# Optimization experiments

Hardware: AMD Instinct MI355X
Metric: run time of the kernel (lower is better)

Reference implementation:

```python
import jax, jax.numpy as jnp
import numpy as np

N, S, H, FA = 16, 64, 256, 256  # batch, sentences, memory_size, fact_attn_hidden


def setup_inputs() -> dict:
    key = jax.random.key(0)
    ks = jax.random.split(key, 12)
    g = lambda k, shp: (jax.random.normal(k, shp, jnp.float32) * 0.05)
    return dict(
        facts=jax.random.normal(ks[0], (N, S, H), jnp.float32),
        prevM=jax.random.normal(ks[1], (N, S, H), jnp.float32),
        questions=jax.random.normal(ks[2], (N, S, H), jnp.float32),
        doc_len=jax.random.randint(ks[3], (N,), S // 2, S + 1),
        z1_w=g(ks[4], (FA, 4 * H)), z1_b=jnp.zeros((FA,), jnp.float32),
        z2_w=g(ks[5], (1, FA)), z2_b=jnp.zeros((1,), jnp.float32),
        Wr_w=g(ks[6], (H, H)), Wr_b=jnp.zeros((H,), jnp.float32),
        Ur_w=g(ks[7], (H, H)), Ur_b=jnp.zeros((H,), jnp.float32),
        W_w=g(ks[8], (H, H)), W_b=jnp.zeros((H,), jnp.float32),
        U_w=g(ks[9], (H, H)), U_b=jnp.zeros((H,), jnp.float32),
        nm_w=g(ks[10], (H, 3 * H)), nm_b=jnp.zeros((H,), jnp.float32),
    )


def reference(facts, prevM, questions, doc_len,
              z1_w, z1_b, z2_w, z2_b,
              Wr_w, Wr_b, Ur_w, Ur_b, W_w, W_b, U_w, U_b,
              nm_w, nm_b):
    n, s, h = facts.shape
    # ---- make_interaction: pairwise features (query axis = dim1, fact/key axis = dim2)
    f = facts[:, None, :, :]       # (N,1,S,H) broadcast over queries
    m = prevM[:, :, None, :]       # (N,S,1,H) broadcast over keys
    q = questions[:, :, None, :]   # (N,S,1,H)
    z = jnp.concatenate([f * q, f * m, jnp.abs(f - q), jnp.abs(f - m)], axis=-1)  # (N,S,S,4H)
    Gh = jnp.tanh(z @ z1_w.T + z1_b)               # (N,S,S,FA)
    G = (Gh @ z2_w.T + z2_b)[..., 0]               # (N,S,S)
    mask = (jnp.arange(s) < doc_len[:, None]).astype(G.dtype)  # (N,S) key mask
    Gm = G * mask[:, None, :]
    Gm = jnp.where(Gm == 0, -jnp.inf, Gm)          # faithful to G[G==0] = -inf
    attn = jax.nn.softmax(Gm, axis=2)              # (N,S,S)

    # ---- AttentionalGRU over the S facts for each of the N*S query rows
    B = n * s
    fb = jnp.broadcast_to(facts[:, None], (n, s, s, h)).reshape(B, s, h)  # (B,S,H)
    gb = attn.reshape(B, s)                                               # (B,S)

    def step(C, xs):
        fact, gt = xs                                   # fact: (B,H), gt: (B,)
        r = jax.nn.sigmoid(fact @ Wr_w.T + Wr_b + C @ Ur_w.T + Ur_b)
        h_t = jnp.tanh(fact @ W_w.T + W_b + r * (C @ U_w.T + U_b))
        gt = gt[:, None]
        return gt * h_t + (1.0 - gt) * C, None

    C0 = jnp.zeros((B, h), facts.dtype)
    C, _ = jax.lax.scan(step, C0, (fb.transpose(1, 0, 2), gb.T))  # scan over S steps
    C = C.reshape(n, s, h)

    # ---- memory update (dropouts are identity in eval mode)
    concat = jnp.concatenate([prevM, C, questions], axis=-1)  # (N,S,3H)
    next_mem = jax.nn.relu(concat @ nm_w.T + nm_b)            # (N,S,H)
    return next_mem, attn
```

## Files before the change

kernel.cpp:

```cpp
#include <hip/hip_runtime.h>
#include <hip/hip_bf16.h>
#include <math.h>

#define NB 16
#define SS 64
#define HH 256
#define FAA 256

using short8 = __attribute__((ext_vector_type(8))) short;
using f32x4  = __attribute__((ext_vector_type(4))) float;

__device__ __forceinline__ unsigned int cvtpk(float a, float b) {
  unsigned int r;
  asm("v_cvt_pk_bf16_f32 %0, %1, %2" : "=v"(r) : "v"(a), "v"(b));
  return r;
}
__device__ __forceinline__ float sel4(const f32x4 a, int q) {
  const float s01 = (q & 1) ? a[1] : a[0];
  const float s23 = (q & 1) ? a[3] : a[2];
  return (q & 2) ? s23 : s01;
}

__global__ __launch_bounds__(256) void prolog_fused(
    const float* __restrict__ z1w, const float* __restrict__ Ur,
    const float* __restrict__ U, const float* __restrict__ nmw,
    const float* __restrict__ pm, const float* __restrict__ qs,
    unsigned short* __restrict__ z1wbf, unsigned short* __restrict__ wcatbf,
    unsigned short* __restrict__ nmbf, unsigned short* __restrict__ pmbf,
    unsigned short* __restrict__ qbf,
    const float* __restrict__ facts, const float* __restrict__ Wr,
    const float* __restrict__ Wrb, const float* __restrict__ Urb,
    const float* __restrict__ Ww, const float* __restrict__ Wb,
    float* __restrict__ FWr, float* __restrict__ FW) {
  __shared__ float fl[4][HH];
  const int bid = blockIdx.x, tid = threadIdx.x;

  auto cvt8 = [&](const float* src, unsigned short* dst, int base) {
    const float4 a = *(const float4*)(src + base);
    const float4 b = *(const float4*)(src + base + 4);
    uint4 o;
    o.x = cvtpk(a.x, a.y); o.y = cvtpk(a.z, a.w);
    o.z = cvtpk(b.x, b.y); o.w = cvtpk(b.z, b.w);
    *(uint4*)(dst + base) = o;
  };
  auto cvt8perm = [&](const float* row, unsigned short* dst, int sbase, int c0) {
    const float4 lo = *(const float4*)(row + c0);
    const float4 hi = *(const float4*)(row + c0 + 16);
    uint4 o;
    o.x = cvtpk(lo.x, hi.x); o.y = cvtpk(lo.y, hi.y);
    o.z = cvtpk(lo.z, hi.z); o.w = cvtpk(lo.w, hi.w);
    *(uint4*)(dst + sbase) = o;
  };

  if (bid < 128) {
    const int base = (bid * 256 + tid) * 8;
    cvt8(z1w, z1wbf, base);
    return;
  }
  if (bid < 192) {
    const int base = ((bid - 128) * 256 + tid) * 8;
    const int o = base >> 8, s0 = base & 255;
    const int gb = s0 & ~31, t0 = s0 & 31;
    const float* row = (o < 256) ? (Ur + o * 256) : (U + (o - 256) * 256);
    cvt8perm(row, wcatbf, base, gb + (t0 >> 1));
    return;
  }
  if (bid < 288) {
    const int base = ((bid - 192) * 256 + tid) * 8;
    const int o = base / 768, k0 = base - o * 768;
    const float* row = nmw + o * 768;
    if (k0 >= 256 && k0 < 512) {
      const int s0 = k0 - 256, gb = s0 & ~31, t0 = s0 & 31;
      cvt8perm(row, nmbf, base, 256 + gb + (t0 >> 1));
    } else {
      cvt8(row, nmbf + o * 768, k0);
    }
    return;
  }
  if (bid < 416) {
    const int base = ((bid - 288) * 256 + tid) * 8;
    cvt8(pm, pmbf, base);
    return;
  }
  if (bid < 544) {
    const int base = ((bid - 416) * 256 + tid) * 8;
    cvt8(qs, qbf, base);
    return;
  }
  const int b0 = (bid - 544) * 4;
#pragma unroll
  for (int r = 0; r < 4; ++r) fl[r][tid] = facts[(b0 + r) * HH + tid];
  __syncthreads();
  float ar[4] = {0.f, 0.f, 0.f, 0.f}, aw[4] = {0.f, 0.f, 0.f, 0.f};
  const float4* wr = (const float4*)(Wr + tid * HH);
  const float4* ww = (const float4*)(Ww + tid * HH);
  for (int d4 = 0; d4 < 64; ++d4) {
    float4 a = wr[d4], b = ww[d4];
#pragma unroll
    for (int r = 0; r < 4; ++r) {
      float4 f = *(const float4*)&fl[r][d4 * 4];
      ar[r] += a.x * f.x + a.y * f.y + a.z * f.z + a.w * f.w;
      aw[r] += b.x * f.x + b.y * f.y + b.z * f.z + b.w * f.w;
    }
  }
  const float br = Wrb[tid] + Urb[tid], bw = Wb[tid];
#pragma unroll
  for (int r = 0; r < 4; ++r) {
    FWr[(b0 + r) * HH + tid] = ar[r] + br;
    FW[(b0 + r) * HH + tid] = aw[r] + bw;
  }
}

__global__ __launch_bounds__(512, 4) void gate_gemm(
    const float* __restrict__ facts, const float* __restrict__ prevM,
    const float* __restrict__ questions, const unsigned short* __restrict__ z1wbf,
    const float* __restrict__ z1b, const float* __restrict__ z2w,
    const float* __restrict__ z2b, const int* __restrict__ doc_len,
    float* __restrict__ attn) {
  __shared__ unsigned short Ab[3][128 * 32];
  __shared__ unsigned short Bb[3][256 * 32];
  __shared__ float Gpart[128][4];

  const int bi = blockIdx.x;
  const int n = bi >> 5, i0 = (bi & 31) * 2;
  const int tid = threadIdx.x;
  const int w = tid >> 6, l = tid & 63;
  const int rg = w >> 2, cg = w & 3;
  const int l15 = l & 15, q = l >> 4;
  const int t15 = tid & 15, jb = tid >> 4;

  const float* fn = facts + n * SS * HH;
  const float* qn = questions + (n * SS + i0) * HH;
  const float* mn = prevM + (n * SS + i0) * HH;

  auto stageB = [&](int buf, int c) {
    const int kb = (c & 3) * 256 + (c >> 2) * 32;
    const int swz = ((l & 3) ^ ((l >> 2) & 3)) * 8;
#pragma unroll
    for (int j = 0; j < 2; ++j) {
      const int colg = w * 32 + j * 16 + (l >> 2);
      const unsigned short* src = z1wbf + colg * 1024 + kb + swz;
      __builtin_amdgcn_global_load_lds(src, Bb[buf] + (w * 32 + j * 16) * 32, 16, 0, 0);
    }
  };

  auto buildA = [&](int buf, int s, float2 f0, float2 f1, float2 q0, float2 q1,
                    float2 m0, float2 m1) {
    unsigned int* dst = (unsigned int*)Ab[buf];
    const int dsw = t15 ^ ((jb & 3) << 2);
    const float2 o0 = (s & 1) ? m0 : q0;
    const float2 o1 = (s & 1) ? m1 : q1;
#pragma unroll
    for (int pl = 0; pl < 2; ++pl) {
      const float fx = pl ? f1.x : f0.x;
      const float fy = pl ? f1.y : f0.y;
#pragma unroll
      for (int il = 0; il < 2; ++il) {
        const int row = il * 64 + pl * 32 + jb;
        const float ox = il ? o1.x : o0.x;
        const float oy = il ? o1.y : o0.y;
        float a, b;
        if (s < 2) { a = fx * ox;         b = fy * oy; }
        else       { a = fabsf(fx - ox);  b = fabsf(fy - oy); }
        dst[row * 16 + dsw] = cvtpk(a, b);
      }
    }
  };

  const f32x4 zero4 = {0.f, 0.f, 0.f, 0.f};
  f32x4 acc[4][4];
#pragma unroll
  for (int a = 0; a < 4; ++a)
#pragma unroll
    for (int b = 0; b < 4; ++b) acc[a][b] = zero4;

  auto mfmaStep = [&](int buf) {
    short8 Bfr[4];
#pragma unroll
    for (int nf = 0; nf < 4; ++nf) {
      const int col = cg * 64 + nf * 16 + l15;
      Bfr[nf] = *(const short8*)&Bb[buf][col * 32 + (q ^ (l15 & 3)) * 8];
    }
    __builtin_amdgcn_s_setprio(1);
#pragma unroll
    for (int mf = 0; mf < 4; ++mf) {
      const int row = rg * 64 + mf * 16 + l15;
      const short8 Afm = *(const short8*)&Ab[buf][row * 32 + (q ^ (l15 & 3)) * 8];
#pragma unroll
      for (int nf = 0; nf < 4; ++nf)
        acc[mf][nf] = __builtin_amdgcn_mfma_f32_16x16x32_bf16(Afm, Bfr[nf], acc[mf][nf], 0, 0, 0);
    }
    __builtin_amdgcn_s_setprio(0);
  };

  const int hh2 = t15 * 2;
  auto pf = [&](int hc, float2& f0, float2& f1, float2& q0, float2& q1,
                float2& m0, float2& m1) {
    const int h = hc * 32 + hh2;
    f0 = *(const float2*)(fn + jb * HH + h);
    f1 = *(const float2*)(fn + (jb + 32) * HH + h);
    q0 = *(const float2*)(qn + h);
    q1 = *(const float2*)(qn + HH + h);
    m0 = *(const float2*)(mn + h);
    m1 = *(const float2*)(mn + HH + h);
  };

  float2 Rf0, Rf1, Rq0, Rq1, Rm0, Rm1;
  float2 Sf0, Sf1, Sq0, Sq1, Sm0, Sm1;
  pf(0, Rf0, Rf1, Rq0, Rq1, Rm0, Rm1);
  stageB(0, 0);
  stageB(1, 1);
  buildA(0, 0, Rf0, Rf1, Rq0, Rq1, Rm0, Rm1);
  asm volatile("s_waitcnt vmcnt(2) lgkmcnt(0)\n\ts_barrier" ::: "memory");

#pragma unroll
  for (int c = 0; c < 32; ++c) {
    const int s = c & 3, hc = c >> 2;
    const int cb = c % 3, nb2 = (c + 1) % 3, fb = (c + 2) % 3;
    const bool pfphase = (s == 2) && (hc < 7);

    if (c + 2 < 32) stageB(fb, c + 2);
    if (pfphase) pf(hc + 1, Sf0, Sf1, Sq0, Sq1, Sm0, Sm1);
    if (c + 1 < 32) {
      if (((c + 1) & 3) == 0)
        buildA(nb2, 0, Sf0, Sf1, Sq0, Sq1, Sm0, Sm1);
      else
        buildA(nb2, (c + 1) & 3, Rf0, Rf1, Rq0, Rq1, Rm0, Rm1);
    }
    mfmaStep(cb);

    if (c <= 29) {
      if (pfphase)
        asm volatile("s_waitcnt vmcnt(8) lgkmcnt(0)\n\ts_barrier" ::: "memory");
      else
        asm volatile("s_waitcnt vmcnt(2) lgkmcnt(0)\n\ts_barrier" ::: "memory");
    } else if (c == 30) {
      asm volatile("s_waitcnt vmcnt(0) lgkmcnt(0)\n\ts_barrier" ::: "memory");
    }
    if (s == 3) {
      Rf0 = Sf0; Rf1 = Sf1; Rq0 = Sq0; Rq1 = Sq1; Rm0 = Sm0; Rm1 = Sm1;
    }
  }

  float psum[4][4];
#pragma unroll
  for (int mf = 0; mf < 4; ++mf)
#pragma unroll
    for (int v = 0; v < 4; ++v) psum[mf][v] = 0.f;

#pragma unroll
  for (int nf = 0; nf < 4; ++nf) {
    const int k = cg * 64 + nf * 16 + l15;
    const float zb = z1b[k], zw = z2w[k];
#pragma unroll
    for (int mf = 0; mf < 4; ++mf)
#pragma unroll
      for (int v = 0; v < 4; ++v) {
        const float x = acc[mf][nf][v] + zb;
        const float e = __expf(2.f * x);
        const float t = 1.f - 2.f / (e + 1.f);
        psum[mf][v] += zw * t;
      }
  }
#pragma unroll
  for (int d = 1; d < 16; d <<= 1)
#pragma unroll
    for (int mf = 0; mf < 4; ++mf)
#pragma unroll
      for (int v = 0; v < 4; ++v) psum[mf][v] += __shfl_xor(psum[mf][v], d, 64);
  if (l15 == 0) {
#pragma unroll
    for (int mf = 0; mf < 4; ++mf)
#pragma unroll
      for (int v = 0; v < 4; ++v)
        Gpart[rg * 64 + mf * 16 + q * 4 + v][cg] = psum[mf][v];
  }
  __syncthreads();
  if (tid < 128) {
    const float gg = Gpart[tid][0] + Gpart[tid][1] + Gpart[tid][2] + Gpart[tid][3] + z2b[0];
    const int i = i0 + (tid >> 6), j = tid & 63;
    const int dl = doc_len[n];
    const float x = (j < dl && gg != 0.0f) ? gg : -INFINITY;
    float mx = x;
#pragma unroll
    for (int d = 1; d < 64; d <<= 1) mx = fmaxf(mx, __shfl_xor(mx, d, 64));
    const float e = (x == -INFINITY) ? 0.f : __expf(x - mx);
    float s = e;
#pragma unroll
    for (int d = 1; d < 64; d <<= 1) s += __shfl_xor(s, d, 64);
    attn[(n * SS + i) * SS + j] = e / s;
  }
}

__global__ __launch_bounds__(512, 2) void gru_scan(
    const unsigned short* __restrict__ wcat, const float* __restrict__ FWr,
    const float* __restrict__ FW, const float* __restrict__ Ub,
    const float* __restrict__ attn, unsigned short* __restrict__ Cout) {
  __shared__ unsigned short Cbf[2][4 * 272];
  __shared__ float attn_sT[64 * 4];

  const int bi = blockIdx.x, n = bi >> 4, i0 = (bi & 15) * 4;
  const int tid = threadIdx.x, w = tid >> 6, l = tid & 63;
  const int l15 = l & 15, q = l >> 4;
  const int h0 = w * 32 + l15;

  short8 Bf[8][4];
#pragma unroll
  for (int f = 0; f < 4; ++f) {
    const int wrow = ((f >> 1) ? 256 : 0) + w * 32 + (f & 1) * 16 + l15;
    const unsigned short* bb = wcat + wrow * 256 + q * 8;
#pragma unroll
    for (int kt = 0; kt < 8; ++kt)
      Bf[kt][f] = *(const short8*)(bb + kt * 32);
  }

  const float ub0 = Ub[h0], ub1 = Ub[h0 + 16];

  for (int e = tid; e < 64 * 4; e += 512)
    attn_sT[e] = attn[(n * SS + i0 + (e & 3)) * SS + (e >> 2)];
  for (int e = tid; e < 544; e += 512)
    ((unsigned int*)Cbf[0])[e] = 0u;
  __syncthreads();

  const float* fwr_g = FWr + n * SS * HH;
  const float* fw_g  = FW + n * SS * HH;

  float cm0 = 0.f, cm1 = 0.f;
  float fr0 = fwr_g[h0], fr1 = fwr_g[h0 + 16];
  float fc0 = fw_g[h0],  fc1 = fw_g[h0 + 16];

  for (int t = 0; t < 64; ++t) {
    const int cur = t & 1;
    const unsigned short* Cr = Cbf[cur];
    unsigned int* Cw = (unsigned int*)Cbf[cur ^ 1];

    short8 Af[8];
    const int arow = (l15 & 3) * 272;
#pragma unroll
    for (int kt = 0; kt < 8; ++kt)
      Af[kt] = *(const short8*)&Cr[arow + kt * 32 + q * 8];

    float nr0 = 0.f, nr1 = 0.f, nc0 = 0.f, nc1 = 0.f;
    if (t < 63) {
      nr0 = fwr_g[(t + 1) * HH + h0];
      nr1 = fwr_g[(t + 1) * HH + h0 + 16];
      nc0 = fw_g[(t + 1) * HH + h0];
      nc1 = fw_g[(t + 1) * HH + h0 + 16];
    }

    const f32x4 z4 = {0.f, 0.f, 0.f, 0.f};
    f32x4 a0 = z4, a1 = z4, a2 = z4, a3 = z4;
    __builtin_amdgcn_s_setprio(1);
#pragma unroll
    for (int kt = 0; kt < 8; ++kt) {
      a0 = __builtin_amdgcn_mfma_f32_16x16x32_bf16(Af[kt], Bf[kt][0], a0, 0, 0, 0);
      a2 = __builtin_amdgcn_mfma_f32_16x16x32_bf16(Af[kt], Bf[kt][2], a2, 0, 0, 0);
    }
#pragma unroll
    for (int kt = 0; kt < 8; ++kt) {
      a1 = __builtin_amdgcn_mfma_f32_16x16x32_bf16(Af[kt], Bf[kt][1], a1, 0, 0, 0);
      a3 = __builtin_amdgcn_mfma_f32_16x16x32_bf16(Af[kt], Bf[kt][3], a3, 0, 0, 0);
    }
    __builtin_amdgcn_s_setprio(0);

    const float g = attn_sT[t * 4 + q];

    const float yr0 = sel4(a0, q), yu0 = sel4(a2, q);
    const float r0 = 1.f / (1.f + __expf(-(fr0 + yr0)));
    const float x0 = fc0 + r0 * (yu0 + ub0);
    const float e0 = __expf(2.f * x0);
    const float h0t = 1.f - 2.f / (e0 + 1.f);
    cm0 += g * (h0t - cm0);

    const float yr1 = sel4(a1, q), yu1 = sel4(a3, q);
    const float r1 = 1.f / (1.f + __expf(-(fr1 + yr1)));
    const float x1 = fc1 + r1 * (yu1 + ub1);
    const float e1 = __expf(2.f * x1);
    const float h1t = 1.f - 2.f / (e1 + 1.f);
    cm1 += g * (h1t - cm1);

    Cw[q * 136 + w * 16 + l15] = cvtpk(cm0, cm1);

    fr0 = nr0; fr1 = nr1; fc0 = nc0; fc1 = nc1;
    __syncthreads();
  }

  {
    const int row = tid >> 7, wo = tid & 127;
    ((unsigned int*)Cout)[(n * SS + i0 + row) * 128 + wo] =
        *(const unsigned int*)&Cbf[0][row * 272 + wo * 2];
  }
}

__global__ __launch_bounds__(256) void next_mem_gemm(
    const unsigned short* __restrict__ pmbf, const unsigned short* __restrict__ cbf,
    const unsigned short* __restrict__ qbf, const unsigned short* __restrict__ nmbf,
    const float* __restrict__ nmb, float* __restrict__ out) {
  __shared__ unsigned short A[64][40];
  const int bi = blockIdx.x;
  const int rb = bi >> 3, cb = bi & 7;
  const int r0 = rb * 64, c0 = cb * 32;
  const int tid = threadIdx.x, w = tid >> 6, l = tid & 63;
  const int l15 = l & 15, q = l >> 4;

  f32x4 acc[2];
  const f32x4 z4 = {0.f, 0.f, 0.f, 0.f};
#pragma unroll
  for (int nf = 0; nf < 2; ++nf) acc[nf] = z4;

  for (int kt = 0; kt < 24; ++kt) {
    const int kg = kt * 32;
    const unsigned short* src =
        kg < 256 ? (pmbf + kg) : (kg < 512 ? (cbf + kg - 256) : (qbf + kg - 512));
    const int kk = (tid & 15) * 2;
#pragma unroll
    for (int ps = 0; ps < 4; ++ps) {
      const int row = ps * 16 + (tid >> 4);
      *(unsigned int*)&A[row][kk] = *(const unsigned int*)(src + (r0 + row) * HH + kk);
    }
    __syncthreads();
    short8 Bfr[2];
#pragma unroll
    for (int nf = 0; nf < 2; ++nf)
      Bfr[nf] = *(const short8*)(nmbf + (c0 + nf * 16 + l15) * 768 + kg + q * 8);
    const short8 Af = *(const short8*)&A[w * 16 + l15][q * 8];
#pragma unroll
    for (int nf = 0; nf < 2; ++nf)
      acc[nf] = __builtin_amdgcn_mfma_f32_16x16x32_bf16(Af, Bfr[nf], acc[nf], 0, 0, 0);
    __syncthreads();
  }
#pragma unroll
  for (int nf = 0; nf < 2; ++nf) {
    const int col = c0 + nf * 16 + l15;
    const float bv = nmb[col];
#pragma unroll
    for (int v = 0; v < 4; ++v) {
      const int grow = r0 + w * 16 + q * 4 + v;
      out[grow * HH + col] = fmaxf(acc[nf][v] + bv, 0.f);
    }
  }
}

extern "C" void kernel_launch(void* const* d_in, const int* in_sizes, int n_in,
                              void* d_out, int out_size, void* d_ws, size_t ws_size,
                              hipStream_t stream) {
  const float* facts     = (const float*)d_in[0];
  const float* prevM     = (const float*)d_in[1];
  const float* questions = (const float*)d_in[2];
  const int*   doc_len   = (const int*)d_in[3];
  const float* z1w = (const float*)d_in[4];
  const float* z1b = (const float*)d_in[5];
  const float* z2w = (const float*)d_in[6];
  const float* z2b = (const float*)d_in[7];
  const float* Wrw = (const float*)d_in[8];
  const float* Wrb = (const float*)d_in[9];
  const float* Urw = (const float*)d_in[10];
  const float* Urb = (const float*)d_in[11];
  const float* Ww  = (const float*)d_in[12];
  const float* Wb  = (const float*)d_in[13];
  const float* Uw  = (const float*)d_in[14];
  const float* Ub  = (const float*)d_in[15];
  const float* nmw = (const float*)d_in[16];
  const float* nmb = (const float*)d_in[17];

  char* ws = (char*)d_ws;
  unsigned short* z1wbf  = (unsigned short*)(ws + 0);
  unsigned short* wcatbf = (unsigned short*)(ws + 524288);
  unsigned short* nmbf   = (unsigned short*)(ws + 786432);
  unsigned short* pmbf   = (unsigned short*)(ws + 1179648);
  unsigned short* qbf    = (unsigned short*)(ws + 1703936);
  float* FWr = (float*)(ws + 2490368);
  float* FW  = (float*)(ws + 3538944);
  unsigned short* cbf = (unsigned short*)(ws + 4587520);

  float* out  = (float*)d_out;
  float* attn = out + NB * SS * HH;

  prolog_fused<<<800, 256, 0, stream>>>(z1w, Urw, Uw, nmw, prevM, questions,
                                        z1wbf, wcatbf, nmbf, pmbf, qbf,
                                        facts, Wrw, Wrb, Urb, Ww, Wb, FWr, FW);
  gate_gemm<<<512, 512, 0, stream>>>(facts, prevM, questions, z1wbf, z1b, z2w, z2b,
                                     doc_len, attn);
  gru_scan<<<256, 512, 0, stream>>>(wcatbf, FWr, FW, Ub, attn, cbf);
  next_mem_gemm<<<128, 256, 0, stream>>>(pmbf, cbf, qbf, nmbf, nmb, out);
}
```

Baseline: 242.1 us.

## Split GRU scan into two launches and drop LDS staging in next-mem GEMM

The 64-step GRU scan is split into two kernel launches of 32 steps each. Per-thread state is saved to workspace between them and reloaded, reusing the z1w and cbf regions. The next_mem GEMM drops its shared-memory A staging and its barriers: it loads MFMA fragments straight from global memory, using 128-thread blocks over 32-row tiles with twice as many blocks. The split adds a launch and a state round-trip with no clear parallelism gain, so it may be a probe. The workspace aliasing relies on cbf being written only after part 1 reads its saved state.

```diff
diff --git a/kernel.cpp b/kernel.cpp
--- a/kernel.cpp
+++ b/kernel.cpp
@@ -295,7 +295,8 @@
 __global__ __launch_bounds__(512, 2) void gru_scan(
     const unsigned short* __restrict__ wcat, const float* __restrict__ FWr,
     const float* __restrict__ FW, const float* __restrict__ Ub,
-    const float* __restrict__ attn, unsigned short* __restrict__ Cout) {
+    const float* __restrict__ attn, unsigned short* __restrict__ Cout,
+    float* __restrict__ cm0save, float* __restrict__ cm1save, const int part) {
   __shared__ unsigned short Cbf[2][4 * 272];
   __shared__ float attn_sT[64 * 4];
 
@@ -318,18 +319,27 @@
 
   for (int e = tid; e < 64 * 4; e += 512)
     attn_sT[e] = attn[(n * SS + i0 + (e & 3)) * SS + (e >> 2)];
-  for (int e = tid; e < 544; e += 512)
-    ((unsigned int*)Cbf[0])[e] = 0u;
+
+  float cm0, cm1;
+  if (part == 0) {
+    for (int e = tid; e < 544; e += 512)
+      ((unsigned int*)Cbf[0])[e] = 0u;
+    cm0 = 0.f; cm1 = 0.f;
+  } else {
+    cm0 = cm0save[bi * 512 + tid];
+    cm1 = cm1save[bi * 512 + tid];
+    ((unsigned int*)Cbf[0])[q * 136 + w * 16 + l15] = cvtpk(cm0, cm1);
+  }
   __syncthreads();
 
   const float* fwr_g = FWr + n * SS * HH;
   const float* fw_g  = FW + n * SS * HH;
 
-  float cm0 = 0.f, cm1 = 0.f;
-  float fr0 = fwr_g[h0], fr1 = fwr_g[h0 + 16];
-  float fc0 = fw_g[h0],  fc1 = fw_g[h0 + 16];
-
-  for (int t = 0; t < 64; ++t) {
+  const int tbeg = part ? 32 : 0, tend = part ? 64 : 32;
+  float fr0 = fwr_g[tbeg * HH + h0], fr1 = fwr_g[tbeg * HH + h0 + 16];
+  float fc0 = fw_g[tbeg * HH + h0],  fc1 = fw_g[tbeg * HH + h0 + 16];
+
+  for (int t = tbeg; t < tend; ++t) {
     const int cur = t & 1;
     const unsigned short* Cr = Cbf[cur];
     unsigned int* Cw = (unsigned int*)Cbf[cur ^ 1];
@@ -385,6 +395,11 @@
     __syncthreads();
   }
 
+  if (part == 0) {
+    cm0save[bi * 512 + tid] = cm0;
+    cm1save[bi * 512 + tid] = cm1;
+    return;
+  }
   {
     const int row = tid >> 7, wo = tid & 127;
     ((unsigned int*)Cout)[(n * SS + i0 + row) * 128 + wo] =
@@ -392,51 +407,56 @@
   }
 }
 
-__global__ __launch_bounds__(256) void next_mem_gemm(
+__global__ __launch_bounds__(128) void next_mem_gemm(
     const unsigned short* __restrict__ pmbf, const unsigned short* __restrict__ cbf,
     const unsigned short* __restrict__ qbf, const unsigned short* __restrict__ nmbf,
     const float* __restrict__ nmb, float* __restrict__ out) {
-  __shared__ unsigned short A[64][40];
   const int bi = blockIdx.x;
   const int rb = bi >> 3, cb = bi & 7;
-  const int r0 = rb * 64, c0 = cb * 32;
+  const int r0 = rb * 32, c0 = cb * 32;
   const int tid = threadIdx.x, w = tid >> 6, l = tid & 63;
   const int l15 = l & 15, q = l >> 4;
 
-  f32x4 acc[2];
+  const int arow = (r0 + w * 16 + l15) * HH + q * 8;
+  const unsigned short* nb = nmbf + (c0 + l15) * 768 + q * 8;
+
   const f32x4 z4 = {0.f, 0.f, 0.f, 0.f};
-#pragma unroll
-  for (int nf = 0; nf < 2; ++nf) acc[nf] = z4;
-
-  for (int kt = 0; kt < 24; ++kt) {
-    const int kg = kt * 32;
-    const unsigned short* src =
-        kg < 256 ? (pmbf + kg) : (kg < 512 ? (cbf + kg - 256) : (qbf + kg - 512));
-    const int kk = (tid & 15) * 2;
-#pragma unroll
-    for (int ps = 0; ps < 4; ++ps) {
-      const int row = ps * 16 + (tid >> 4);
-      *(unsigned int*)&A[row][kk] = *(const unsigned int*)(src + (r0 + row) * HH + kk);
-    }
-    __syncthreads();
-    short8 Bfr[2];
-#pragma unroll
-    for (int nf = 0; nf < 2; ++nf)
-      Bfr[nf] = *(const short8*)(nmbf + (c0 + nf * 16 + l15) * 768 + kg + q * 8);
-    const short8 Af = *(const short8*)&A[w * 16 + l15][q * 8];
-#pragma unroll
-    for (int nf = 0; nf < 2; ++nf)
-      acc[nf] = __builtin_amdgcn_mfma_f32_16x16x32_bf16(Af, Bfr[nf], acc[nf], 0, 0, 0);
-    __syncthreads();
-  }
+  f32x4 acc0 = z4, acc1 = z4;
+
+#pragma unroll
+  for (int kt = 0; kt < 8; ++kt) {
+    const short8 Af = *(const short8*)(pmbf + arow + kt * 32);
+    const short8 B0 = *(const short8*)(nb + kt * 32);
+    const short8 B1 = *(const short8*)(nb + 16 * 768 + kt * 32);
+    acc0 = __builtin_amdgcn_mfma_f32_16x16x32_bf16(Af, B0, acc0, 0, 0, 0);
+    acc1 = __builtin_amdgcn_mfma_f32_16x16x32_bf16(Af, B1, acc1, 0, 0, 0);
+  }
+#pragma unroll
+  for (int kt = 0; kt < 8; ++kt) {
+    const short8 Af = *(const short8*)(cbf + arow + kt * 32);
+    const short8 B0 = *(const short8*)(nb + 256 + kt * 32);
+    const short8 B1 = *(const short8*)(nb + 16 * 768 + 256 + kt * 32);
+    acc0 = __builtin_amdgcn_mfma_f32_16x16x32_bf16(Af, B0, acc0, 0, 0, 0);
+    acc1 = __builtin_amdgcn_mfma_f32_16x16x32_bf16(Af, B1, acc1, 0, 0, 0);
+  }
+#pragma unroll
+  for (int kt = 0; kt < 8; ++kt) {
+    const short8 Af = *(const short8*)(qbf + arow + kt * 32);
+    const short8 B0 = *(const short8*)(nb + 512 + kt * 32);
+    const short8 B1 = *(const short8*)(nb + 16 * 768 + 512 + kt * 32);
+    acc0 = __builtin_amdgcn_mfma_f32_16x16x32_bf16(Af, B0, acc0, 0, 0, 0);
+    acc1 = __builtin_amdgcn_mfma_f32_16x16x32_bf16(Af, B1, acc1, 0, 0, 0);
+  }
+
 #pragma unroll
   for (int nf = 0; nf < 2; ++nf) {
     const int col = c0 + nf * 16 + l15;
     const float bv = nmb[col];
+    const f32x4 a = nf ? acc1 : acc0;
 #pragma unroll
     for (int v = 0; v < 4; ++v) {
       const int grow = r0 + w * 16 + q * 4 + v;
-      out[grow * HH + col] = fmaxf(acc[nf][v] + bv, 0.f);
+      out[grow * HH + col] = fmaxf(a[v] + bv, 0.f);
     }
   }
 }
@@ -473,6 +493,9 @@
   float* FW  = (float*)(ws + 3538944);
   unsigned short* cbf = (unsigned short*)(ws + 4587520);
 
+  float* cm0save = (float*)(ws + 0);
+  float* cm1save = (float*)(ws + 4587520);
+
   float* out  = (float*)d_out;
   float* attn = out + NB * SS * HH;
 
@@ -481,6 +504,7 @@
                                         facts, Wrw, Wrb, Urb, Ww, Wb, FWr, FW);
   gate_gemm<<<512, 512, 0, stream>>>(facts, prevM, questions, z1wbf, z1b, z2w, z2b,
                                      doc_len, attn);
-  gru_scan<<<256, 512, 0, stream>>>(wcatbf, FWr, FW, Ub, attn, cbf);
-  next_mem_gemm<<<128, 256, 0, stream>>>(pmbf, cbf, qbf, nmbf, nmb, out);
-}
+  gru_scan<<<256, 512, 0, stream>>>(wcatbf, FWr, FW, Ub, attn, cbf, cm0save, cm1save, 0);
+  gru_scan<<<256, 512, 0, stream>>>(wcatbf, FWr, FW, Ub, attn, cbf, cm0save, cm1save, 1);
+  next_mem_gemm<<<256, 128, 0, stream>>>(pmbf, cbf, qbf, nmbf, nmb, out);
+}
```

Result: no change. 241.1 us (-0.4%).
